# Kernel tuning notes

Measured on AMD Instinct MI355X. Metric: run time of the kernel, lower is better.

The kernel has to match this reference:

```python
import jax, jax.numpy as jnp
import numpy as np

V_EN = 50000; V_FR = 50000; D = 256; B = 64; S = 64; NEG = 8192; PAD = 0


def setup_inputs() -> dict:
    key = jax.random.key(0)
    k = jax.random.split(key, 8)
    zs = jax.random.normal(k[0], (B, S, D), dtype=jnp.float32) * 0.1
    x_en = jax.random.randint(k[1], (B, S), 1, V_EN)  # avoid pad row 0
    x_fr = jax.random.randint(k[2], (B, S), 1, V_FR)
    en_mask = jnp.ones((B, S), dtype=jnp.float32)
    fr_mask = jnp.ones((B, S), dtype=jnp.float32)
    W_en = jax.random.normal(k[3], (V_EN, D), dtype=jnp.float32) * 0.05
    W_en = W_en.at[PAD].set(0.0)  # padding_idx row is zero
    W_fr = jax.random.normal(k[4], (V_FR, D), dtype=jnp.float32) * 0.05
    W_fr = W_fr.at[PAD].set(0.0)
    # Host-side CSS sampling, mirroring the torch module's numpy/multinomial step.
    rng = np.random.default_rng(0)
    pos_en = np.unique(np.asarray(x_en))
    neg_en = rng.choice(np.setdiff1d(np.arange(V_EN), pos_en), NEG, replace=False)
    kappa_en = jnp.float32((V_EN - pos_en.shape[0]) / NEG)
    pos_fr = np.unique(np.asarray(x_fr))
    neg_fr = rng.choice(np.setdiff1d(np.arange(V_FR), pos_fr), NEG, replace=False)
    kappa_fr = jnp.float32((V_FR - pos_fr.shape[0]) / NEG)
    return {
        "zs": zs, "x_en": x_en, "x_fr": x_fr,
        "en_mask": en_mask, "fr_mask": fr_mask,
        "W_en": W_en, "W_fr": W_fr,
        "pos_en": jnp.asarray(pos_en), "neg_en": jnp.asarray(neg_en),
        "pos_fr": jnp.asarray(pos_fr), "neg_fr": jnp.asarray(neg_fr),
        "kappa_en": kappa_en, "kappa_fr": kappa_fr,
    }


def _css_denom(zs, W, pos_idx, neg_idx, kappa):
    # zs: [B,S,D]; pos/neg embeddings: [P,D]/[N,D] -> denom [B,S]
    pos_e = W[pos_idx]
    neg_e = W[neg_idx]
    pos_score = jnp.exp(jnp.einsum("bsd,pd->bsp", zs, pos_e)).sum(-1)
    neg_score = kappa * jnp.exp(jnp.einsum("bsd,nd->bsn", zs, neg_e)).sum(-1)
    return pos_score + neg_score


def reference(zs, x_en, x_fr, en_mask, fr_mask, W_en, W_fr,
              pos_en, neg_en, pos_fr, neg_fr, kappa_en, kappa_fr):
    # --- English CSS: per-token score ---
    be_en = W_en[x_en]                                   # [B,S,D]
    en_batch = jnp.exp((zs * be_en).sum(-1))             # [B,S]
    en_probs = en_batch / _css_denom(zs, W_en, pos_en, neg_en, kappa_en)
    # --- French CSS: alignment score against every en position ---
    be_fr = W_fr[x_fr]                                   # [B,Sf,D]
    fr_batch = jnp.exp(jnp.einsum("bfd,bsd->bfs", be_fr, zs))  # [B,Sf,S]
    fr_denom = _css_denom(zs, W_fr, pos_fr, neg_fr, kappa_fr)  # [B,S]
    fr_probs = fr_batch / fr_denom[:, None, :]
    en_rec_loss = (jnp.log(en_probs) * en_mask).sum(axis=1)            # [B]
    fr_rec_loss = (jnp.log(fr_probs.sum(axis=2)) * fr_mask).sum(axis=1)  # [B]
    return en_rec_loss, fr_rec_loss
```

## Files before the change

kernel.cpp:

```cpp
#include <hip/hip_runtime.h>

#define DDIM 256
#define NTOK 4096
#define NEGN 8192
#define TM 64
#define TN 64
#define LDT 40

typedef __attribute__((ext_vector_type(8))) short bf16x8;
typedef __attribute__((ext_vector_type(4))) float f32x4;

__device__ inline unsigned short f2bf(float f) {
    unsigned int u = __float_as_uint(f);
    unsigned int r = u + 0x7FFFu + ((u >> 16) & 1u);
    return (unsigned short)(r >> 16);
}

__device__ inline void gl_lds16(const unsigned short* g, unsigned short* l) {
    __builtin_amdgcn_global_load_lds(
        reinterpret_cast<__attribute__((address_space(1))) unsigned int*>(
            reinterpret_cast<uintptr_t>(g)),
        reinterpret_cast<__attribute__((address_space(3))) unsigned int*>(
            reinterpret_cast<uintptr_t>(l)),
        16, 0, 0);
}

__device__ inline void wait_vmcnt4() { asm volatile("s_waitcnt vmcnt(4)" ::: "memory"); }
__device__ inline void wait_vmcnt2() { asm volatile("s_waitcnt vmcnt(2)" ::: "memory"); }
__device__ inline void wait_vmcnt0() { asm volatile("s_waitcnt vmcnt(0)" ::: "memory"); }
__device__ inline void raw_barrier() { asm volatile("s_barrier" ::: "memory"); }

template<int CTRL>
__device__ inline float dpp_add(float x) {
    int v = __builtin_amdgcn_update_dpp(0, __float_as_int(x), CTRL, 0xF, 0xF, false);
    return x + __int_as_float(v);
}
__device__ inline float red16(float x) {
    x = dpp_add<0xB1>(x);
    x = dpp_add<0x4E>(x);
    x = dpp_add<0x141>(x);
    x = dpp_add<0x140>(x);
    return x;
}

__global__ void gather_kernel(
    const float* __restrict__ zs,
    const float* __restrict__ W_en, const float* __restrict__ W_fr,
    const int* __restrict__ pos_en, const int* __restrict__ neg_en,
    const int* __restrict__ pos_fr, const int* __restrict__ neg_fr,
    const int* __restrict__ x_en,
    const float* __restrict__ kappa_en, const float* __restrict__ kappa_fr,
    unsigned short* __restrict__ z_bf,
    unsigned short* __restrict__ E_en, unsigned short* __restrict__ E_fr,
    float* __restrict__ w_en, float* __restrict__ w_fr,
    float* __restrict__ en_score,
    float* __restrict__ denom_en, float* __restrict__ denom_fr,
    int Pe, int Pf, int Lpe, int Lpf)
{
    int row  = blockIdx.x * 4 + (threadIdx.x >> 6);
    int lane = threadIdx.x & 63;
    const float* src = nullptr;
    unsigned short* dst = nullptr;
    bool zero = false;

    if (row < NTOK) {
        src = zs + (size_t)row * DDIM;
        dst = z_bf + (size_t)row * DDIM;
        if (lane == 0) { denom_en[row] = 0.0f; denom_fr[row] = 0.0f; }
    } else if (row < NTOK + Lpe) {
        int j = row - NTOK;
        int Le = Pe + NEGN;
        int idx = 0;
        if (j < Pe)      idx = pos_en[j];
        else if (j < Le) idx = neg_en[j - Pe];
        else             zero = true;
        src = W_en + (size_t)idx * DDIM;
        dst = E_en + (size_t)j * DDIM;
        if (lane == 0) w_en[j] = (j < Pe) ? 1.0f : (j < Le ? kappa_en[0] : 0.0f);
    } else if (row < NTOK + Lpe + Lpf) {
        int j = row - NTOK - Lpe;
        int Lf = Pf + NEGN;
        int idx = 0;
        if (j < Pf)      idx = pos_fr[j];
        else if (j < Lf) idx = neg_fr[j - Pf];
        else             zero = true;
        src = W_fr + (size_t)idx * DDIM;
        dst = E_fr + (size_t)j * DDIM;
        if (lane == 0) w_fr[j] = (j < Pf) ? 1.0f : (j < Lf ? kappa_fr[0] : 0.0f);
    } else if (row < NTOK + Lpe + Lpf + NTOK) {
        int j = row - NTOK - Lpe - Lpf;
        int idx = x_en[j];
        float4 z = *(const float4*)(zs   + (size_t)j   * DDIM + lane * 4);
        float4 w = *(const float4*)(W_en + (size_t)idx * DDIM + lane * 4);
        float s = z.x * w.x + z.y * w.y + z.z * w.z + z.w * w.w;
        #pragma unroll
        for (int m = 32; m; m >>= 1) s += __shfl_xor(s, m);
        if (lane == 0) en_score[j] = s;
        return;
    } else {
        return;
    }

    int d = lane * 4;
    float4 v;
    if (zero) { v.x = v.y = v.z = v.w = 0.0f; }
    else      { v = *(const float4*)(src + d); }
    ushort4 o;
    o.x = f2bf(v.x); o.y = f2bf(v.y); o.z = f2bf(v.z); o.w = f2bf(v.w);
    *(ushort4*)(dst + d) = o;
}

__global__ __launch_bounds__(256, 2) void expsum_stream(
    const unsigned short* __restrict__ A,
    const unsigned short* __restrict__ E,
    const float* __restrict__ wts,
    float* __restrict__ out_en, float* __restrict__ out_fr,
    int Lpe, int NT)
{
    __shared__ __align__(16) unsigned short Bs[4][4096];

    int fid = blockIdx.y * 32 + blockIdx.x;
    int xcd = fid & 7;
    int r   = fid >> 3;
    int yb  = xcd * 2 + (r & 1);
    int xb  = r >> 1;

    int t    = threadIdx.x;
    int lane = t & 63;
    int wave = t >> 6;
    int col  = lane & 15;
    int quad = lane >> 4;
    int wm   = wave & 1;
    int wn   = wave >> 1;

    bf16x8 afr[4][8];
    {
        const unsigned short* Ap =
            A + ((size_t)(xb * 128 + wm * 64 + col)) * DDIM + quad * 8;
        #pragma unroll
        for (int i = 0; i < 4; i++)
            #pragma unroll
            for (int c = 0; c < 8; c++)
                afr[i][c] = *(const bf16x8*)(Ap + (size_t)i * 16 * DDIM + c * 32);
    }

    float sums[4][4];
    #pragma unroll
    for (int i = 0; i < 4; i++)
        #pragma unroll
        for (int rr = 0; rr < 4; rr++) sums[i][rr] = 0.0f;
    float* curout = out_en;
    int outrow = xb * 128 + wm * 64;

    int ntiles = (NT - yb + 15) >> 4;

    {
        const unsigned short* g0 =
            E + (size_t)(yb * 128 + 32 * wave + col) * DDIM + quad * 8;
        gl_lds16(g0,                 &Bs[0][wave * 1024]);
        gl_lds16(g0 + 16 * DDIM,     &Bs[0][wave * 1024 + 512]);
        gl_lds16(g0 + 32,            &Bs[1][wave * 1024]);
        gl_lds16(g0 + 16 * DDIM + 32,&Bs[1][wave * 1024 + 512]);
    }

    for (int s = 0; s < ntiles; s++) {
        int tl = yb + (s << 4);
        int nb = tl * 128;
        bool last = (s == ntiles - 1);

        float wj[4];
        #pragma unroll
        for (int j = 0; j < 4; j++)
            wj[j] = wts[nb + wn * 64 + 16 * j + col];

        float* o = (nb >= Lpe) ? out_fr : out_en;
        if (o != curout) {
            if (col == 0) {
                #pragma unroll
                for (int i = 0; i < 4; i++)
                    #pragma unroll
                    for (int rr = 0; rr < 4; rr++)
                        atomicAdd(curout + outrow + 16 * i + quad * 4 + rr, sums[i][rr]);
            }
            #pragma unroll
            for (int i = 0; i < 4; i++)
                #pragma unroll
                for (int rr = 0; rr < 4; rr++) sums[i][rr] = 0.0f;
            curout = o;
        }

        f32x4 acc[4][4];
        #pragma unroll
        for (int i = 0; i < 4; i++)
            #pragma unroll
            for (int j = 0; j < 4; j++)
                acc[i][j] = (f32x4){0.f, 0.f, 0.f, 0.f};

        #pragma unroll
        for (int k8 = 0; k8 < 8; k8++) {
            int rb = k8 & 3;
            int rs = (k8 + 2) & 3;
            if (!last || k8 < 6) {
                int c2  = s * 8 + k8 + 2;
                int tl2 = yb + ((c2 >> 3) << 4);
                int kk2 = (c2 & 7) * 32;
                const unsigned short* g =
                    E + (size_t)(tl2 * 128 + 32 * wave + col) * DDIM + kk2 + quad * 8;
                gl_lds16(g,             &Bs[rs][wave * 1024]);
                gl_lds16(g + 16 * DDIM, &Bs[rs][wave * 1024 + 512]);
                wait_vmcnt4();
            } else if (k8 == 6) {
                wait_vmcnt2();
            } else {
                wait_vmcnt0();
            }
            raw_barrier();

            bf16x8 bfv[4];
            #pragma unroll
            for (int j = 0; j < 4; j++)
                bfv[j] = *(const bf16x8*)(&Bs[rb][(wn * 4 + j) * 512 + quad * 128 + col * 8]);
            #pragma unroll
            for (int j = 0; j < 4; j++)
                #pragma unroll
                for (int i = 0; i < 4; i++)
                    acc[i][j] = __builtin_amdgcn_mfma_f32_16x16x32_bf16(
                        afr[i][k8], bfv[j], acc[i][j], 0, 0, 0);
        }

        #pragma unroll
        for (int i = 0; i < 4; i++)
            #pragma unroll
            for (int rr = 0; rr < 4; rr++) {
                float sv = wj[0] * __expf(acc[i][0][rr]) + wj[1] * __expf(acc[i][1][rr])
                         + wj[2] * __expf(acc[i][2][rr]) + wj[3] * __expf(acc[i][3][rr]);
                sums[i][rr] += red16(sv);
            }
    }

    if (col == 0) {
        #pragma unroll
        for (int i = 0; i < 4; i++)
            #pragma unroll
            for (int rr = 0; rr < 4; rr++)
                atomicAdd(curout + outrow + 16 * i + quad * 4 + rr, sums[i][rr]);
    }
}

__global__ __launch_bounds__(256) void expsum_gemm64_loss(
    const float* __restrict__ W_fr,
    const int* __restrict__ x_fr,
    const unsigned short* __restrict__ Bm,
    const float* __restrict__ denom_fr,
    const float* __restrict__ denom_en,
    const float* __restrict__ en_score,
    const float* __restrict__ en_mask,
    const float* __restrict__ fr_mask,
    float* __restrict__ outloss)
{
    __shared__ __align__(16) unsigned short lda[TM * LDT];
    __shared__ __align__(16) unsigned short ldb[TN * LDT];
    __shared__ float tbuf[64];

    int batch = blockIdx.x;
    const unsigned short* Bb = Bm + (size_t)batch * TN * DDIM;

    int t      = threadIdx.x;
    int srow   = t >> 2;
    int schunk = t & 3;
    int lane   = t & 63;
    int wave   = t >> 6;
    int col    = lane & 15;
    int quad   = lane >> 4;

    int aidx = x_fr[batch * 64 + srow];
    const float* Arow = W_fr + (size_t)aidx * DDIM;

    f32x4 acc0 = {0.f,0.f,0.f,0.f};
    f32x4 acc1 = {0.f,0.f,0.f,0.f};
    f32x4 acc2 = {0.f,0.f,0.f,0.f};
    f32x4 acc3 = {0.f,0.f,0.f,0.f};

    for (int kk = 0; kk < DDIM; kk += 32) {
        float4 f0 = *(const float4*)(Arow + kk + schunk * 8);
        float4 f1 = *(const float4*)(Arow + kk + schunk * 8 + 4);
        uint4 bv = *(const uint4*)(Bb + (size_t)srow * DDIM + kk + schunk * 8);
        ushort4 ua; ua.x = f2bf(f0.x); ua.y = f2bf(f0.y); ua.z = f2bf(f0.z); ua.w = f2bf(f0.w);
        ushort4 ub; ub.x = f2bf(f1.x); ub.y = f2bf(f1.y); ub.z = f2bf(f1.z); ub.w = f2bf(f1.w);
        __syncthreads();
        *(ushort4*)(lda + srow * LDT + schunk * 8)     = ua;
        *(ushort4*)(lda + srow * LDT + schunk * 8 + 4) = ub;
        *(uint4*)(ldb + srow * LDT + schunk * 8) = bv;
        __syncthreads();

        bf16x8 af = *(const bf16x8*)(lda + (wave * 16 + col) * LDT + quad * 8);
        bf16x8 b0 = *(const bf16x8*)(ldb + ( 0 + col) * LDT + quad * 8);
        bf16x8 b1 = *(const bf16x8*)(ldb + (16 + col) * LDT + quad * 8);
        bf16x8 b2 = *(const bf16x8*)(ldb + (32 + col) * LDT + quad * 8);
        bf16x8 b3 = *(const bf16x8*)(ldb + (48 + col) * LDT + quad * 8);
        acc0 = __builtin_amdgcn_mfma_f32_16x16x32_bf16(af, b0, acc0, 0, 0, 0);
        acc1 = __builtin_amdgcn_mfma_f32_16x16x32_bf16(af, b1, acc1, 0, 0, 0);
        acc2 = __builtin_amdgcn_mfma_f32_16x16x32_bf16(af, b2, acc2, 0, 0, 0);
        acc3 = __builtin_amdgcn_mfma_f32_16x16x32_bf16(af, b3, acc3, 0, 0, 0);
    }

    const float* db = denom_fr + batch * 64;
    float w0 = 1.0f / db[ 0 + col];
    float w1 = 1.0f / db[16 + col];
    float w2 = 1.0f / db[32 + col];
    float w3 = 1.0f / db[48 + col];

    float tot0 = w0 * __expf(acc0.x) + w1 * __expf(acc1.x) + w2 * __expf(acc2.x) + w3 * __expf(acc3.x);
    float tot1 = w0 * __expf(acc0.y) + w1 * __expf(acc1.y) + w2 * __expf(acc2.y) + w3 * __expf(acc3.y);
    float tot2 = w0 * __expf(acc0.z) + w1 * __expf(acc1.z) + w2 * __expf(acc2.z) + w3 * __expf(acc3.z);
    float tot3 = w0 * __expf(acc0.w) + w1 * __expf(acc1.w) + w2 * __expf(acc2.w) + w3 * __expf(acc3.w);

    #pragma unroll
    for (int m = 1; m < 16; m <<= 1) {
        tot0 += __shfl_xor(tot0, m);
        tot1 += __shfl_xor(tot1, m);
        tot2 += __shfl_xor(tot2, m);
        tot3 += __shfl_xor(tot3, m);
    }
    if (col == 0) {
        int base = wave * 16 + quad * 4;
        tbuf[base + 0] = tot0; tbuf[base + 1] = tot1;
        tbuf[base + 2] = tot2; tbuf[base + 3] = tot3;
    }
    __syncthreads();

    if (t < 64) {
        int i = batch * 64 + t;
        float a = (en_score[i] - __logf(denom_en[i])) * en_mask[i];
        float c = __logf(tbuf[t]) * fr_mask[i];
        #pragma unroll
        for (int m = 32; m; m >>= 1) { a += __shfl_xor(a, m); c += __shfl_xor(c, m); }
        if (t == 0) { outloss[batch] = a; outloss[64 + batch] = c; }
    }
}

extern "C" void kernel_launch(void* const* d_in, const int* in_sizes, int n_in,
                              void* d_out, int out_size, void* d_ws, size_t ws_size,
                              hipStream_t stream)
{
    const float* zs       = (const float*)d_in[0];
    const int*   x_en     = (const int*)d_in[1];
    const int*   x_fr     = (const int*)d_in[2];
    const float* en_mask  = (const float*)d_in[3];
    const float* fr_mask  = (const float*)d_in[4];
    const float* W_en     = (const float*)d_in[5];
    const float* W_fr     = (const float*)d_in[6];
    const int*   pos_en   = (const int*)d_in[7];
    const int*   neg_en   = (const int*)d_in[8];
    const int*   pos_fr   = (const int*)d_in[9];
    const int*   neg_fr   = (const int*)d_in[10];
    const float* kappa_en = (const float*)d_in[11];
    const float* kappa_fr = (const float*)d_in[12];

    int Pe  = in_sizes[7];
    int Pf  = in_sizes[9];
    int Lpe = (Pe + NEGN + 127) & ~127;
    int Lpf = (Pf + NEGN + 127) & ~127;
    int Ltot = Lpe + Lpf;
    int NT   = Ltot / 128;

    char* w = (char*)d_ws;
    float* denom_en = (float*)w; w += NTOK * 4;
    float* denom_fr = (float*)w; w += NTOK * 4;
    float* en_score = (float*)w; w += NTOK * 4;
    float* w_all    = (float*)w; w += (size_t)Ltot * 4;
    unsigned short* z_bf  = (unsigned short*)w; w += (size_t)NTOK * DDIM * 2;
    unsigned short* E_all = (unsigned short*)w; w += (size_t)Ltot * DDIM * 2;

    int totrows = NTOK + Lpe + Lpf + NTOK;
    gather_kernel<<<(totrows + 3) / 4, 256, 0, stream>>>(
        zs, W_en, W_fr, pos_en, neg_en, pos_fr, neg_fr, x_en,
        kappa_en, kappa_fr, z_bf, E_all, E_all + (size_t)Lpe * DDIM,
        w_all, w_all + Lpe, en_score, denom_en, denom_fr, Pe, Pf, Lpe, Lpf);

    expsum_stream<<<dim3(32, 16), 256, 0, stream>>>(
        z_bf, E_all, w_all, denom_en, denom_fr, Lpe, NT);

    expsum_gemm64_loss<<<64, 256, 0, stream>>>(
        W_fr, x_fr, z_bf, denom_fr, denom_en, en_score, en_mask, fr_mask,
        (float*)d_out);
}
```

Baseline: 208.8 us.

## Give each wave private LDS staging to drop block barriers in expsum stream

The streaming exp-sum GEMM now gives each wave its own slice of LDS and its own 64 embedding rows per 256-row tile. Each wave stages its own data through a 4-deep buffer and waits only on its own vmcnt, so the per-k-step block barrier is gone. Block tiling changes from 128x128 with a 2x2 wave split to 64 tokens x 256 embeddings, and the launch grid becomes 64x8 without the XCD swizzle. The per-embedding weights are computed inline from Pe/Pf and kappa instead of being written and read from a workspace array. The trade-off is that each wave now reloads the A-side z rows with less sharing, and the smaller M tile lowers MFMA reuse of the B data across waves.

```diff
diff --git a/kernel.cpp b/kernel.cpp
--- a/kernel.cpp
+++ b/kernel.cpp
@@ -25,10 +25,9 @@
         16, 0, 0);
 }
 
+__device__ inline void wait_vmcnt8() { asm volatile("s_waitcnt vmcnt(8)" ::: "memory"); }
 __device__ inline void wait_vmcnt4() { asm volatile("s_waitcnt vmcnt(4)" ::: "memory"); }
-__device__ inline void wait_vmcnt2() { asm volatile("s_waitcnt vmcnt(2)" ::: "memory"); }
 __device__ inline void wait_vmcnt0() { asm volatile("s_waitcnt vmcnt(0)" ::: "memory"); }
-__device__ inline void raw_barrier() { asm volatile("s_barrier" ::: "memory"); }
 
 template<int CTRL>
 __device__ inline float dpp_add(float x) {
@@ -49,10 +48,8 @@
     const int* __restrict__ pos_en, const int* __restrict__ neg_en,
     const int* __restrict__ pos_fr, const int* __restrict__ neg_fr,
     const int* __restrict__ x_en,
-    const float* __restrict__ kappa_en, const float* __restrict__ kappa_fr,
     unsigned short* __restrict__ z_bf,
     unsigned short* __restrict__ E_en, unsigned short* __restrict__ E_fr,
-    float* __restrict__ w_en, float* __restrict__ w_fr,
     float* __restrict__ en_score,
     float* __restrict__ denom_en, float* __restrict__ denom_fr,
     int Pe, int Pf, int Lpe, int Lpf)
@@ -76,7 +73,6 @@
         else             zero = true;
         src = W_en + (size_t)idx * DDIM;
         dst = E_en + (size_t)j * DDIM;
-        if (lane == 0) w_en[j] = (j < Pe) ? 1.0f : (j < Le ? kappa_en[0] : 0.0f);
     } else if (row < NTOK + Lpe + Lpf) {
         int j = row - NTOK - Lpe;
         int Lf = Pf + NEGN;
@@ -86,7 +82,6 @@
         else             zero = true;
         src = W_fr + (size_t)idx * DDIM;
         dst = E_fr + (size_t)j * DDIM;
-        if (lane == 0) w_fr[j] = (j < Pf) ? 1.0f : (j < Lf ? kappa_fr[0] : 0.0f);
     } else if (row < NTOK + Lpe + Lpf + NTOK) {
         int j = row - NTOK - Lpe - Lpf;
         int idx = x_en[j];
@@ -113,30 +108,28 @@
 __global__ __launch_bounds__(256, 2) void expsum_stream(
     const unsigned short* __restrict__ A,
     const unsigned short* __restrict__ E,
-    const float* __restrict__ wts,
+    const float* __restrict__ kep, const float* __restrict__ kfp,
     float* __restrict__ out_en, float* __restrict__ out_fr,
-    int Lpe, int NT)
+    int Pe, int Pf, int Lpe, int NT)
 {
-    __shared__ __align__(16) unsigned short Bs[4][4096];
-
-    int fid = blockIdx.y * 32 + blockIdx.x;
-    int xcd = fid & 7;
-    int r   = fid >> 3;
-    int yb  = xcd * 2 + (r & 1);
-    int xb  = r >> 1;
+    __shared__ __align__(16) unsigned short Bs[4][4][2048];
+
+    int lin = blockIdx.y * 64 + blockIdx.x;
+    int yb  = lin & 7;
+    int xb  = lin >> 3;
 
     int t    = threadIdx.x;
     int lane = t & 63;
     int wave = t >> 6;
     int col  = lane & 15;
     int quad = lane >> 4;
-    int wm   = wave & 1;
-    int wn   = wave >> 1;
+
+    float ke = kep[0], kf = kfp[0];
+    asm volatile("" : "+v"(ke), "+v"(kf) : : "memory");
 
     bf16x8 afr[4][8];
     {
-        const unsigned short* Ap =
-            A + ((size_t)(xb * 128 + wm * 64 + col)) * DDIM + quad * 8;
+        const unsigned short* Ap = A + ((size_t)(xb * 64 + col)) * DDIM + quad * 8;
         #pragma unroll
         for (int i = 0; i < 4; i++)
             #pragma unroll
@@ -150,28 +143,31 @@
         #pragma unroll
         for (int rr = 0; rr < 4; rr++) sums[i][rr] = 0.0f;
     float* curout = out_en;
-    int outrow = xb * 128 + wm * 64;
-
-    int ntiles = (NT - yb + 15) >> 4;
-
-    {
-        const unsigned short* g0 =
-            E + (size_t)(yb * 128 + 32 * wave + col) * DDIM + quad * 8;
-        gl_lds16(g0,                 &Bs[0][wave * 1024]);
-        gl_lds16(g0 + 16 * DDIM,     &Bs[0][wave * 1024 + 512]);
-        gl_lds16(g0 + 32,            &Bs[1][wave * 1024]);
-        gl_lds16(g0 + 16 * DDIM + 32,&Bs[1][wave * 1024 + 512]);
-    }
+    int outrow = xb * 64;
+
+    int ntiles = (NT - yb + 7) >> 3;
+    int C = ntiles * 8;
+    unsigned short* myBs = &Bs[wave][0][0];
+
+    #define STAGE(c) do {                                                     \
+        int tl_ = yb + (((c) >> 3) << 3);                                     \
+        int kk_ = ((c) & 7) * 32;                                             \
+        int ngb_ = tl_ * 256 + wave * 64;                                     \
+        const unsigned short* g_ =                                            \
+            E + (size_t)(ngb_ + col) * DDIM + kk_ + quad * 8;                 \
+        unsigned short* l_ = myBs + ((c) & 3) * 2048;                         \
+        gl_lds16(g_,                 l_);                                     \
+        gl_lds16(g_ + 16 * DDIM,     l_ + 512);                               \
+        gl_lds16(g_ + 32 * DDIM,     l_ + 1024);                              \
+        gl_lds16(g_ + 48 * DDIM,     l_ + 1536);                              \
+    } while (0)
+
+    STAGE(0);
+    STAGE(1);
 
     for (int s = 0; s < ntiles; s++) {
-        int tl = yb + (s << 4);
-        int nb = tl * 128;
-        bool last = (s == ntiles - 1);
-
-        float wj[4];
-        #pragma unroll
-        for (int j = 0; j < 4; j++)
-            wj[j] = wts[nb + wn * 64 + 16 * j + col];
+        int tl = yb + (s << 3);
+        int nb = tl * 256;
 
         float* o = (nb >= Lpe) ? out_fr : out_en;
         if (o != curout) {
@@ -189,6 +185,18 @@
             curout = o;
         }
 
+        float wj[4];
+        #pragma unroll
+        for (int j = 0; j < 4; j++) {
+            int ngl = nb + wave * 64 + 16 * j + col;
+            if (nb < Lpe) {
+                wj[j] = (ngl < Pe) ? 1.0f : ((ngl < Pe + NEGN) ? ke : 0.0f);
+            } else {
+                int nl = ngl - Lpe;
+                wj[j] = (nl < Pf) ? 1.0f : ((nl < Pf + NEGN) ? kf : 0.0f);
+            }
+        }
+
         f32x4 acc[4][4];
         #pragma unroll
         for (int i = 0; i < 4; i++)
@@ -198,28 +206,21 @@
 
         #pragma unroll
         for (int k8 = 0; k8 < 8; k8++) {
-            int rb = k8 & 3;
-            int rs = (k8 + 2) & 3;
-            if (!last || k8 < 6) {
-                int c2  = s * 8 + k8 + 2;
-                int tl2 = yb + ((c2 >> 3) << 4);
-                int kk2 = (c2 & 7) * 32;
-                const unsigned short* g =
-                    E + (size_t)(tl2 * 128 + 32 * wave + col) * DDIM + kk2 + quad * 8;
-                gl_lds16(g,             &Bs[rs][wave * 1024]);
-                gl_lds16(g + 16 * DDIM, &Bs[rs][wave * 1024 + 512]);
+            int c  = s * 8 + k8;
+            int rb = c & 3;
+            if (c + 2 < C) {
+                STAGE(c + 2);
+                wait_vmcnt8();
+            } else if (c + 1 < C) {
                 wait_vmcnt4();
-            } else if (k8 == 6) {
-                wait_vmcnt2();
             } else {
                 wait_vmcnt0();
             }
-            raw_barrier();
 
             bf16x8 bfv[4];
             #pragma unroll
             for (int j = 0; j < 4; j++)
-                bfv[j] = *(const bf16x8*)(&Bs[rb][(wn * 4 + j) * 512 + quad * 128 + col * 8]);
+                bfv[j] = *(const bf16x8*)(myBs + rb * 2048 + j * 512 + quad * 128 + col * 8);
             #pragma unroll
             for (int j = 0; j < 4; j++)
                 #pragma unroll
@@ -237,6 +238,7 @@
                 sums[i][rr] += red16(sv);
             }
     }
+    #undef STAGE
 
     if (col == 0) {
         #pragma unroll
@@ -359,27 +361,26 @@
 
     int Pe  = in_sizes[7];
     int Pf  = in_sizes[9];
-    int Lpe = (Pe + NEGN + 127) & ~127;
-    int Lpf = (Pf + NEGN + 127) & ~127;
+    int Lpe = (Pe + NEGN + 255) & ~255;
+    int Lpf = (Pf + NEGN + 255) & ~255;
     int Ltot = Lpe + Lpf;
-    int NT   = Ltot / 128;
+    int NT   = Ltot / 256;
 
     char* w = (char*)d_ws;
     float* denom_en = (float*)w; w += NTOK * 4;
     float* denom_fr = (float*)w; w += NTOK * 4;
     float* en_score = (float*)w; w += NTOK * 4;
-    float* w_all    = (float*)w; w += (size_t)Ltot * 4;
     unsigned short* z_bf  = (unsigned short*)w; w += (size_t)NTOK * DDIM * 2;
     unsigned short* E_all = (unsigned short*)w; w += (size_t)Ltot * DDIM * 2;
 
     int totrows = NTOK + Lpe + Lpf + NTOK;
     gather_kernel<<<(totrows + 3) / 4, 256, 0, stream>>>(
         zs, W_en, W_fr, pos_en, neg_en, pos_fr, neg_fr, x_en,
-        kappa_en, kappa_fr, z_bf, E_all, E_all + (size_t)Lpe * DDIM,
-        w_all, w_all + Lpe, en_score, denom_en, denom_fr, Pe, Pf, Lpe, Lpf);
-
-    expsum_stream<<<dim3(32, 16), 256, 0, stream>>>(
-        z_bf, E_all, w_all, denom_en, denom_fr, Lpe, NT);
+        z_bf, E_all, E_all + (size_t)Lpe * DDIM,
+        en_score, denom_en, denom_fr, Pe, Pf, Lpe, Lpf);
+
+    expsum_stream<<<dim3(64, 8), 256, 0, stream>>>(
+        z_bf, E_all, kappa_en, kappa_fr, denom_en, denom_fr, Pe, Pf, Lpe, NT);
 
     expsum_gemm64_loss<<<64, 256, 0, stream>>>(
         W_fr, x_fr, z_bf, denom_fr, denom_en, en_score, en_mask, fr_mask,
```

Measured after the change: 248.8 us. 1.19x slower.
